# Kernel optimization log

Hardware: AMD Instinct MI355X
Metric: run time of the kernel (lower is better)

## Reference

```python
import jax, jax.numpy as jnp
import numpy as np

R, T, N, S = 64, 256, 1024, 2  # runs, timesteps, agents, sensing dim


def setup_inputs() -> dict:
    key = jax.random.key(0)
    k_runs, k_comm, k_w1, k_b1, k_w2, k_b2 = jax.random.split(key, 6)
    runs = jax.random.normal(k_runs, (R, T, N, S), dtype=jnp.float32)
    comm0 = jax.random.uniform(k_comm, (R, N), dtype=jnp.float32)  # init_comm middle entries ~ U(0,1)
    # SNet params: Linear(4,10) -> tanh -> Linear(10,2)
    w1 = jax.random.normal(k_w1, (10, 4), dtype=jnp.float32) * 0.5
    b1 = jax.random.normal(k_b1, (10,), dtype=jnp.float32) * 0.1
    w2 = jax.random.normal(k_w2, (2, 10), dtype=jnp.float32) * 0.5
    b2 = jax.random.normal(k_b2, (2,), dtype=jnp.float32) * 0.1
    return {"runs": runs, "comm0": comm0, "w1": w1, "b1": b1, "w2": w2, "b2": b2}


def reference(runs, comm0, w1, b1, w2, b2):
    # runs: (R, T, N, 2); comm0: (R, N)
    n = runs.shape[2]
    # comm vector is (N+2,) with zero boundary cells at both ends (init_comm)
    comm_init = jnp.pad(comm0, ((0, 0), (1, 1)))  # (R, N+2)
    idx = jnp.arange(n)

    def agent_step(comm, inp_i):
        i, x = inp_i  # i: scalar agent index, x: (2,) sensing
        inp = jnp.concatenate([x, jnp.stack([comm[i], comm[i + 2]])])  # (4,)
        h = jnp.tanh(w1 @ inp + b1)
        out = w2 @ h + b2  # (2,): [control, comm_update]
        comm = comm.at[i + 1].set(out[1])
        return comm, out[0]

    def time_step(comm, xs):
        # xs: (N, 2); sequential left-to-right scan over agents (Sync.sequential)
        comm, controls = jax.lax.scan(agent_step, comm, (idx, xs))
        return comm, controls  # controls: (N,)

    def run_fn(comm_row, run):
        # run: (T, N, 2); comm persists across timesteps within a run
        _, controls = jax.lax.scan(time_step, comm_row, run)
        return controls  # (T, N)

    return jax.vmap(run_fn)(comm_init, runs)  # (R, T, N)
```

## Files before the change

kernel.cpp:

```cpp
#include <hip/hip_runtime.h>

#define RR 64
#define TT 256
#define NN 1024
#define CC 32
#define RB 128
#define NSTEP 51
#define C0SZ 1648

typedef float v2f __attribute__((ext_vector_type(2)));

extern "C" __global__ __launch_bounds__(256, 1)
void comnet_kernel(const float* __restrict__ runs,
                   const float* __restrict__ comm0,
                   const float* __restrict__ w1,
                   const float* __restrict__ b1,
                   const float* __restrict__ w2,
                   const float* __restrict__ b2,
                   float* __restrict__ out)
{
    const int r    = blockIdx.x;
    const int t    = threadIdx.x;
    const int lane = t & 63;
    const int wv   = t >> 6;
    const int skew = 2 * t + wv * CC;

    __shared__ __attribute__((aligned(16))) float s_c0[C0SZ];
    __shared__ __attribute__((aligned(16))) float s_ring[4][RB];

    for (int k = t; k < C0SZ; k += 256) {
        float v = 0.0f;
        if (k >= 3 && k < 3 + NN) v = comm0[r * NN + (k - 3)];
        s_c0[k] = v;
    }

    const float Kc = 2.885390081777927f;
    v2f Ax[5], Ay[5], Al[5], Ar[5], Bz[5], M0[5], M1[5];
    float C0 = b2[0], C1 = b2[1];
#pragma unroll
    for (int j = 0; j < 5; ++j) {
        const int k0 = 2 * j, k1 = 2 * j + 1;
        Ax[j] = v2f{Kc * w1[k0 * 4 + 0], Kc * w1[k1 * 4 + 0]};
        Ay[j] = v2f{Kc * w1[k0 * 4 + 1], Kc * w1[k1 * 4 + 1]};
        Al[j] = v2f{Kc * w1[k0 * 4 + 2], Kc * w1[k1 * 4 + 2]};
        Ar[j] = v2f{Kc * w1[k0 * 4 + 3], Kc * w1[k1 * 4 + 3]};
        Bz[j] = v2f{Kc * b1[k0], Kc * b1[k1]};
        const float u00 = w2[k0],      u01 = w2[k1];
        const float u10 = w2[10 + k0], u11 = w2[10 + k1];
        C0 += u00 + u01;
        C1 += u10 + u11;
        M0[j] = v2f{-2.0f * u00, -2.0f * u01};
        M1[j] = v2f{-2.0f * u10, -2.0f * u11};
    }

    __syncthreads();

    const float4* xp4 = (const float4*)(runs + (size_t)(r * TT + t) * NN * 2);
    float*        op  = out + (size_t)(r * TT + t) * NN;

    const bool l0  = (lane == 0);
    const bool l63 = (lane == 63);
    float c_prev = 0.0f;

    auto shr1 = [](float x) {
        const int xi = __float_as_int(x);
        return __int_as_float(__builtin_amdgcn_update_dpp(xi, xi, 0x138, 0xF, 0xF, false));
    };

    auto mlp = [&](float left, float right, float xx, float xy, float& o0) {
        const v2f xv = {xx, xx}, yv = {xy, xy}, lv = {left, left}, rv = {right, right};
        const v2f two = {2.0f, 2.0f};
        v2f acc0 = {0.0f, 0.0f}, acc1 = {0.0f, 0.0f};
#pragma unroll
        for (int j = 0; j < 5; ++j) {
            v2f z = __builtin_elementwise_fma(Ax[j], xv, Bz[j]);
            z = __builtin_elementwise_fma(Ay[j], yv, z);
            z = __builtin_elementwise_fma(Al[j], lv, z);
            z = __builtin_elementwise_fma(Ar[j], rv, z);
            v2f e;
            e.x = __builtin_amdgcn_exp2f(z.x);
            e.y = __builtin_amdgcn_exp2f(z.y);
            const v2f d = e + 1.0f;
            v2f sg;
            sg.x = __builtin_amdgcn_rcpf(d.x);
            sg.y = __builtin_amdgcn_rcpf(d.y);
            const v2f nr = __builtin_elementwise_fma(-d, sg, two);
            sg = sg * nr;
            acc0 = __builtin_elementwise_fma(M0[j], sg, acc0);
            acc1 = __builtin_elementwise_fma(M1[j], sg, acc1);
        }
        o0     = C0 + (acc0.x + acc0.y);
        c_prev = C1 + (acc1.x + acc1.y);
    };

    float4 qc[16];
#pragma unroll
    for (int u = 0; u < 16; ++u) {
        const int idx = min(max(2 * u - skew, 0), NN - 2);
        qc[u] = xp4[idx >> 1];
    }

#pragma unroll 1
    for (int s = 0; s < NSTEP; ++s) {
        const int wbase = s * CC;

        const float4* rbase = (wv == 0)
            ? (const float4*)(s_c0 + (wbase + 4))
            : (const float4*)(s_ring[wv - 1] + (wbase & (RB - 1)));
        float4 rv4[8];
#pragma unroll
        for (int m = 0; m < 8; ++m) rv4[m] = rbase[m];

        float4 qn[16];
        const int i0n = wbase + CC - skew;
#pragma unroll
        for (int u = 0; u < 16; ++u) {
            const int idx = min(max(i0n + 2 * u, 0), NN - 2);
            qn[u] = xp4[idx >> 1];
        }

        const int woff = (wbase + 33) & (RB - 1);
        float* wrow = s_ring[wv];

#pragma unroll
        for (int u = 0; u < 16; ++u) {
            const int  i0  = wbase + 2 * u - skew;
            const bool act = (unsigned)i0 < NN;
            const float rvA = (u & 1) ? rv4[u >> 1].z : rv4[u >> 1].x;
            const float rvB = (u & 1) ? rv4[u >> 1].w : rv4[u >> 1].y;

            float o0a = 0.0f, o0b = 0.0f;

            float nb = shr1(c_prev);
            nb = l0 ? rvA : nb;
            if (act) {
                const float left = (i0 == 0) ? 0.0f : c_prev;
                mlp(left, nb, qc[u].x, qc[u].y, o0a);
            }
            if (l63) wrow[(woff + 2 * u) & (RB - 1)] = c_prev;

            float nb2 = shr1(c_prev);
            nb2 = l0 ? rvB : nb2;
            if (act) {
                const float right = (i0 == NN - 2) ? 0.0f : nb2;
                mlp(c_prev, right, qc[u].z, qc[u].w, o0b);
                *(float2*)(op + i0) = make_float2(o0a, o0b);
            }
            if (l63) wrow[(woff + 2 * u + 1) & (RB - 1)] = c_prev;
        }

#pragma unroll
        for (int u = 0; u < 16; ++u) qc[u] = qn[u];

        __syncthreads();
    }
}

extern "C" void kernel_launch(void* const* d_in, const int* in_sizes, int n_in,
                              void* d_out, int out_size, void* d_ws, size_t ws_size,
                              hipStream_t stream) {
    const float* runs  = (const float*)d_in[0];
    const float* comm0 = (const float*)d_in[1];
    const float* w1    = (const float*)d_in[2];
    const float* b1    = (const float*)d_in[3];
    const float* w2    = (const float*)d_in[4];
    const float* b2    = (const float*)d_in[5];
    float* out = (float*)d_out;
    (void)in_sizes; (void)n_in; (void)out_size; (void)d_ws; (void)ws_size;

    comnet_kernel<<<dim3(RR), dim3(256), 0, stream>>>(runs, comm0, w1, b1, w2, b2, out);
}
```

Measured before the change: 704.2 us.

## Hoist input-dependent MLP terms off the serial comm dependency chain

Precomputes the sensing-input part of the first layer (Ax*x + Ay*y + Bz) for both agents of a pair before the dependent neighbour values arrive, so only two FMAs per hidden pair remain on the sequential chain. It also drops the Newton refinement after the reciprocal and splits the output accumulators into two chains to shorten latency. Ring writes from lane 63 are merged and limited to active steps, and output addressing is simplified. The approximate reciprocal slightly lowers accuracy, and the zb arrays add register pressure.

```diff
diff --git a/kernel.cpp b/kernel.cpp
--- a/kernel.cpp
+++ b/kernel.cpp
@@ -56,7 +56,7 @@
     __syncthreads();
 
     const float4* xp4 = (const float4*)(runs + (size_t)(r * TT + t) * NN * 2);
-    float*        op  = out + (size_t)(r * TT + t) * NN;
+    float*        opb = out + (size_t)(r * TT + t) * NN - skew;
 
     const bool l0  = (lane == 0);
     const bool l63 = (lane == 63);
@@ -67,16 +67,13 @@
         return __int_as_float(__builtin_amdgcn_update_dpp(xi, xi, 0x138, 0xF, 0xF, false));
     };
 
-    auto mlp = [&](float left, float right, float xx, float xy, float& o0) {
-        const v2f xv = {xx, xx}, yv = {xy, xy}, lv = {left, left}, rv = {right, right};
-        const v2f two = {2.0f, 2.0f};
-        v2f acc0 = {0.0f, 0.0f}, acc1 = {0.0f, 0.0f};
+    auto mlp = [&](const v2f* zb, float left, float right, float& o0) {
+        const v2f lv = {left, left}, rv = {right, right};
+        v2f a0a = {0.f, 0.f}, a0b = {0.f, 0.f}, a1a = {0.f, 0.f}, a1b = {0.f, 0.f};
 #pragma unroll
         for (int j = 0; j < 5; ++j) {
-            v2f z = __builtin_elementwise_fma(Ax[j], xv, Bz[j]);
-            z = __builtin_elementwise_fma(Ay[j], yv, z);
-            z = __builtin_elementwise_fma(Al[j], lv, z);
-            z = __builtin_elementwise_fma(Ar[j], rv, z);
+            v2f z = __builtin_elementwise_fma(
+                        Al[j], lv, __builtin_elementwise_fma(Ar[j], rv, zb[j]));
             v2f e;
             e.x = __builtin_amdgcn_exp2f(z.x);
             e.y = __builtin_amdgcn_exp2f(z.y);
@@ -84,13 +81,17 @@
             v2f sg;
             sg.x = __builtin_amdgcn_rcpf(d.x);
             sg.y = __builtin_amdgcn_rcpf(d.y);
-            const v2f nr = __builtin_elementwise_fma(-d, sg, two);
-            sg = sg * nr;
-            acc0 = __builtin_elementwise_fma(M0[j], sg, acc0);
-            acc1 = __builtin_elementwise_fma(M1[j], sg, acc1);
+            if (j < 3) {
+                a0a = __builtin_elementwise_fma(M0[j], sg, a0a);
+                a1a = __builtin_elementwise_fma(M1[j], sg, a1a);
+            } else {
+                a0b = __builtin_elementwise_fma(M0[j], sg, a0b);
+                a1b = __builtin_elementwise_fma(M1[j], sg, a1b);
+            }
         }
-        o0     = C0 + (acc0.x + acc0.y);
-        c_prev = C1 + (acc1.x + acc1.y);
+        const v2f s0 = a0a + a0b, s1 = a1a + a1b;
+        o0     = C0 + (s0.x + s0.y);
+        c_prev = C1 + (s1.x + s1.y);
     };
 
     float4 qc[16];
@@ -119,8 +120,11 @@
             qn[u] = xp4[idx >> 1];
         }
 
+        asm volatile("" ::: "memory");
+
         const int woff = (wbase + 33) & (RB - 1);
         float* wrow = s_ring[wv];
+        float* ops  = opb + wbase;
 
 #pragma unroll
         for (int u = 0; u < 16; ++u) {
@@ -129,24 +133,39 @@
             const float rvA = (u & 1) ? rv4[u >> 1].z : rv4[u >> 1].x;
             const float rvB = (u & 1) ? rv4[u >> 1].w : rv4[u >> 1].y;
 
-            float o0a = 0.0f, o0b = 0.0f;
+            float o0a = 0.0f, o0b, rA = 0.0f;
+            v2f zb1[5];
 
             float nb = shr1(c_prev);
             nb = l0 ? rvA : nb;
             if (act) {
+                v2f zb0[5];
+                const v2f xv0 = {qc[u].x, qc[u].x}, yv0 = {qc[u].y, qc[u].y};
+                const v2f xv1 = {qc[u].z, qc[u].z}, yv1 = {qc[u].w, qc[u].w};
+#pragma unroll
+                for (int j = 0; j < 5; ++j) {
+                    zb0[j] = __builtin_elementwise_fma(
+                                Ay[j], yv0, __builtin_elementwise_fma(Ax[j], xv0, Bz[j]));
+                    zb1[j] = __builtin_elementwise_fma(
+                                Ay[j], yv1, __builtin_elementwise_fma(Ax[j], xv1, Bz[j]));
+                }
                 const float left = (i0 == 0) ? 0.0f : c_prev;
-                mlp(left, nb, qc[u].x, qc[u].y, o0a);
+                mlp(zb0, left, nb, o0a);
+                rA = c_prev;
             }
-            if (l63) wrow[(woff + 2 * u) & (RB - 1)] = c_prev;
 
             float nb2 = shr1(c_prev);
             nb2 = l0 ? rvB : nb2;
             if (act) {
                 const float right = (i0 == NN - 2) ? 0.0f : nb2;
-                mlp(c_prev, right, qc[u].z, qc[u].w, o0b);
-                *(float2*)(op + i0) = make_float2(o0a, o0b);
+                mlp(zb1, c_prev, right, o0b);
+                *(float2*)(ops + 2 * u) = make_float2(o0a, o0b);
             }
-            if (l63) wrow[(woff + 2 * u + 1) & (RB - 1)] = c_prev;
+
+            if (act & l63) {
+                wrow[(woff + 2 * u)     & (RB - 1)] = rA;
+                wrow[(woff + 2 * u + 1) & (RB - 1)] = c_prev;
+            }
         }
 
 #pragma unroll
```

After: 682.8 us. 3.0% less time.
